# Performance work log

Hardware: AMD Instinct MI355X
Metric: run time of the kernel (lower is better)

The kernel has to match this reference:

```python
import jax, jax.numpy as jnp
import numpy as np

H = 2048   # hidden_size
L = 512    # latent_dim
B, S = 4, 2048

def setup_inputs() -> dict:
    key = jax.random.key(0)
    ks = jax.random.split(key, 13)
    def lin(k, fan_in, shape):
        bound = 1.0 / np.sqrt(fan_in)
        return jax.random.uniform(k, shape, jnp.float32, -bound, bound)
    return {
        "hidden_states": jax.random.normal(ks[0], (B, S, H), jnp.float32),
        "num_reasoning_steps": 8,
        # to_latent: Linear(H, 2L) -> ReLU -> Linear(2L, L)
        "W_enc1": lin(ks[1], H, (2 * L, H)), "b_enc1": lin(ks[2], H, (2 * L,)),
        "W_enc2": lin(ks[3], 2 * L, (L, 2 * L)), "b_enc2": lin(ks[4], 2 * L, (L,)),
        # from_latent: Linear(L, 2L) -> ReLU -> Linear(2L, H)
        "W_dec1": lin(ks[5], L, (2 * L, L)), "b_dec1": lin(ks[6], L, (2 * L,)),
        "W_dec2": lin(ks[7], 2 * L, (H, 2 * L)), "b_dec2": lin(ks[8], 2 * L, (H,)),
        # GRUCell(L, L): weight_ih/hh [3L, L], bias_ih/hh [3L]
        "w_ih": lin(ks[9], L, (3 * L, L)), "w_hh": lin(ks[10], L, (3 * L, L)),
        "b_ih": lin(ks[11], L, (3 * L,)), "b_hh": lin(ks[12], L, (3 * L,)),
    }

def _gru_cell(x, h, w_ih, w_hh, b_ih, b_hh):
    # PyTorch GRUCell semantics
    gi = x @ w_ih.T + b_ih   # [*, 3L]
    gh = h @ w_hh.T + b_hh
    i_r, i_z, i_n = jnp.split(gi, 3, axis=-1)
    h_r, h_z, h_n = jnp.split(gh, 3, axis=-1)
    r = jax.nn.sigmoid(i_r + h_r)
    z = jax.nn.sigmoid(i_z + h_z)
    n = jnp.tanh(i_n + r * h_n)
    return (1.0 - z) * n + z * h

def reference(hidden_states, num_reasoning_steps, W_enc1, b_enc1, W_enc2, b_enc2,
              W_dec1, b_dec1, W_dec2, b_dec2, w_ih, w_hh, b_ih, b_hh):
    # encode to latent
    latent = jax.nn.relu(hidden_states @ W_enc1.T + b_enc1) @ W_enc2.T + b_enc2  # [B,S,L]

    def step(lat, _):
        lat = _gru_cell(lat, lat, w_ih, w_hh, b_ih, b_hh)
        return lat, lat

    latent, traj = jax.lax.scan(step, latent, None, length=num_reasoning_steps)
    # traj: [steps, B, S, L] -> [B, S, steps, L]
    latent_trajectory = jnp.transpose(traj, (1, 2, 0, 3))
    decoded = jax.nn.relu(latent @ W_dec1.T + b_dec1) @ W_dec2.T + b_dec2  # [B,S,H]
    return decoded, latent_trajectory
```

## Files before the change

### kernel.cpp

```cpp
#include <hip/hip_runtime.h>
#include <hip/hip_bf16.h>
#include <cstdint>
#include <cstddef>

#define TOKENS   8192
#define HID      2048
#define LAT      512
#define LAT2     1024
#define GCOLS    2048
#define STEPS    8
#define DEC_ELEMS (TOKENS*HID)

typedef __attribute__((ext_vector_type(8))) __bf16 bf16x8;
typedef __attribute__((ext_vector_type(4))) float  f32x4;

__device__ __forceinline__ unsigned short f32_to_bf16_rne(float f) {
  unsigned int u = __float_as_uint(f);
  unsigned int r = (u + 0x7FFFu + ((u >> 16) & 1u)) >> 16;
  return (unsigned short)r;
}
__device__ __forceinline__ float bf16_to_f32(unsigned short u) {
  return __uint_as_float(((unsigned int)u) << 16);
}

__device__ __forceinline__ float sigmoidf_(float x) {
  if (x >= 0.f) { float e = __expf(-x); return 1.f / (1.f + e); }
  float e = __expf(x); return e / (1.f + e);
}
__device__ __forceinline__ float tanhf_(float x) {
  float ax = fabsf(x);
  float e  = __expf(-2.f * ax);
  float t  = (1.f - e) / (1.f + e);
  return copysignf(t, x);
}

__device__ __forceinline__ void gl_lds16(const void* g, void* l) {
  __builtin_amdgcn_global_load_lds(
      (const __attribute__((address_space(1))) void*)g,
      (__attribute__((address_space(3))) void*)l, 16, 0, 0);
}

__global__ void k_cast(const float* __restrict__ s, unsigned short* __restrict__ d, int n4) {
  int i = blockIdx.x * blockDim.x + threadIdx.x;
  int stride = gridDim.x * blockDim.x;
  for (; i < n4; i += stride) {
    float4 v = ((const float4*)s)[i];
    ushort4 o;
    o.x = f32_to_bf16_rne(v.x);
    o.y = f32_to_bf16_rne(v.y);
    o.z = f32_to_bf16_rne(v.z);
    o.w = f32_to_bf16_rne(v.w);
    ((ushort4*)d)[i] = o;
  }
}

__global__ void k_gru_pack(const float* __restrict__ wih, const float* __restrict__ whh,
                           const float* __restrict__ bih, const float* __restrict__ bhh,
                           unsigned short* __restrict__ Wg, float* __restrict__ biasg) {
  int gc = blockIdx.x;
  int l  = gc >> 2;
  int g  = gc & 3;
  int row = (g == 0) ? l : (g == 1) ? (512 + l) : (1024 + l);
  for (int c = threadIdx.x; c < LAT; c += blockDim.x) {
    float v;
    if (g <= 1)      v = wih[row * LAT + c] + whh[row * LAT + c];
    else if (g == 2) v = wih[row * LAT + c];
    else             v = whh[row * LAT + c];
    Wg[(size_t)gc * LAT + c] = f32_to_bf16_rne(v);
  }
  if (threadIdx.x == 0) {
    float b;
    if (g <= 1)      b = bih[row] + bhh[row];
    else if (g == 2) b = bih[row];
    else             b = bhh[row];
    biasg[gc] = b;
  }
}

#define MWG 128
#define NWG 128
#define KTILE 64

template <int EPI>
__global__ __launch_bounds__(256)
void gemm_bt(const unsigned short* __restrict__ A,
             const unsigned short* __restrict__ W,
             const float* __restrict__ bias,
             int K, int N,
             float* __restrict__ outF,
             unsigned short* __restrict__ outB) {
  __shared__ __align__(16) char smem[2 * MWG * KTILE * 2];
  unsigned short* As = (unsigned short*)smem;
  unsigned short* Bs = As + MWG * KTILE;

  const int tid  = threadIdx.x;
  const int lane = tid & 63;
  const int wv   = tid >> 6;
  const int wr   = wv >> 1;
  const int wc   = wv & 1;
  const int m0   = blockIdx.x * MWG;
  const int n0   = blockIdx.y * NWG;

  const int lr = lane & 15;
  const int lq = lane >> 4;

  const int srow = lane >> 3;
  const int scol = (lane & 7) * 8;

  f32x4 acc[4][4];
#pragma unroll
  for (int i = 0; i < 4; ++i)
#pragma unroll
    for (int j = 0; j < 4; ++j) acc[i][j] = (f32x4){0.f, 0.f, 0.f, 0.f};

  const unsigned short* Ab = A + (size_t)m0 * K;
  const unsigned short* Wb = W + (size_t)n0 * K;

  const int KT = K / KTILE;
  for (int kt = 0; kt < KT; ++kt) {
    const int k0 = kt * KTILE;
#pragma unroll
    for (int q = 0; q < 4; ++q) {
      int row = 32 * wv + 8 * q + srow;
      gl_lds16(Ab + (size_t)row * K + k0 + scol, As + (32 * wv + 8 * q) * KTILE);
      gl_lds16(Wb + (size_t)row * K + k0 + scol, Bs + (32 * wv + 8 * q) * KTILE);
    }
    __syncthreads();
#pragma unroll
    for (int kk = 0; kk < KTILE; kk += 32) {
      bf16x8 af[4], bf[4];
#pragma unroll
      for (int i = 0; i < 4; ++i)
        af[i] = *(const bf16x8*)(As + (wr * 64 + i * 16 + lr) * KTILE + kk + lq * 8);
#pragma unroll
      for (int j = 0; j < 4; ++j)
        bf[j] = *(const bf16x8*)(Bs + (wc * 64 + j * 16 + lr) * KTILE + kk + lq * 8);
#pragma unroll
      for (int i = 0; i < 4; ++i)
#pragma unroll
        for (int j = 0; j < 4; ++j)
          acc[i][j] = __builtin_amdgcn_mfma_f32_16x16x32_bf16(af[i], bf[j], acc[i][j], 0, 0, 0);
    }
    __syncthreads();
  }

  float bj[4];
#pragma unroll
  for (int j = 0; j < 4; ++j) bj[j] = bias[n0 + wc * 64 + j * 16 + lr];
#pragma unroll
  for (int i = 0; i < 4; ++i) {
#pragma unroll
    for (int ii = 0; ii < 4; ++ii) {
      int row = m0 + wr * 64 + i * 16 + 4 * lq + ii;
#pragma unroll
      for (int j = 0; j < 4; ++j) {
        int col = n0 + wc * 64 + j * 16 + lr;
        float v = acc[i][j][ii] + bj[j];
        if constexpr (EPI == 0) {
          outB[(size_t)row * N + col] = f32_to_bf16_rne(fmaxf(v, 0.f));
        } else if constexpr (EPI == 1) {
          outB[(size_t)row * N + col] = f32_to_bf16_rne(v);
        } else {
          outF[(size_t)row * N + col] = v;
        }
      }
    }
  }
}


#define WAIT_LGKM0() asm volatile("s_waitcnt lgkmcnt(0)" ::: "memory")
#define WAIT_VM(n)   asm volatile("s_waitcnt vmcnt(" #n ")" ::: "memory")

#define LOAD_A(buf, mh) { \
  const int baseA = (buf)*65536 + wm*16384; \
  _Pragma("unroll") for (int m4 = 0; m4 < 4; ++m4) \
  _Pragma("unroll") for (int kki = 0; kki < 2; ++kki) { \
    int rl = (mh)*64 + m4*16 + lr; \
    int off = (rl*128 + kki*64 + lq*16) ^ ((rl & 7) << 4); \
    aR[mh][m4][kki] = *(const bf16x8*)(lds_ + baseA + off); } }

#define LOAD_B(buf, nh) { \
  const int baseB = (buf)*65536 + 32768 + (wn >> 1)*16384; \
  _Pragma("unroll") for (int n2 = 0; n2 < 2; ++n2) \
  _Pragma("unroll") for (int kki = 0; kki < 2; ++kki) { \
    int rl = (wn & 1)*64 + ((nh)*2 + n2)*16 + lr; \
    int off = (rl*128 + kki*64 + lq*16) ^ ((rl & 7) << 4); \
    bR[nh][n2][kki] = *(const bf16x8*)(lds_ + baseB + off); } }

#define STAGE_A(buf, half, kt) { \
  const unsigned short* gp = A + (size_t)(m0 + (half)*128 + rr8)*K + (size_t)(kt)*64 + cc8; \
  char* dp = lds_ + (buf)*65536 + (half)*16384 + (wv << 10); \
  gl_lds16(gp, dp); \
  gl_lds16(gp + (size_t)64*K, dp + 8192); }

#define STAGE_B(buf, half, kt) { \
  const unsigned short* gp = W + (size_t)(n0 + (half)*128 + rr8)*K + (size_t)(kt)*64 + cc8; \
  char* dp = lds_ + (buf)*65536 + 32768 + (half)*16384 + (wv << 10); \
  gl_lds16(gp, dp); \
  gl_lds16(gp + (size_t)64*K, dp + 8192); }

#define MFMAQ(mh, nh) \
  _Pragma("unroll") for (int kki = 0; kki < 2; ++kki) \
  _Pragma("unroll") for (int n2 = 0; n2 < 2; ++n2) \
  _Pragma("unroll") for (int m4 = 0; m4 < 4; ++m4) \
    acc[(mh)*4 + m4][(nh)*2 + n2] = __builtin_amdgcn_mfma_f32_16x16x32_bf16( \
        aR[mh][m4][kki], bR[nh][n2][kki], acc[(mh)*4 + m4][(nh)*2 + n2], 0, 0, 0);

#define PH_CORE(mh, nh) \
  __builtin_amdgcn_s_barrier(); \
  WAIT_LGKM0(); \
  __builtin_amdgcn_sched_barrier(0); \
  __builtin_amdgcn_s_setprio(1); \
  MFMAQ(mh, nh); \
  __builtin_amdgcn_sched_barrier(0); \
  __builtin_amdgcn_s_setprio(0);

#define PH_BAR() __builtin_amdgcn_s_barrier();

template <int EPI>
__global__ __launch_bounds__(512, 2)
void gemm256(const unsigned short* __restrict__ A,
             const unsigned short* __restrict__ W,
             const float* __restrict__ bias,
             int K, int N, int Ntiles,
             float* __restrict__ outF,
             unsigned short* __restrict__ outB,
             const unsigned short* __restrict__ hInB,
             float* __restrict__ traj,
             int step) {
  __shared__ __align__(16) char lds_[131072];

  const int tid  = threadIdx.x;
  const int lane = tid & 63;
  const int wv   = tid >> 6;
  const int wm   = wv >> 2;
  const int wn   = wv & 3;
  const int lr   = lane & 15;
  const int lq   = lane >> 4;

  const int rr8 = (wv << 3) + (lane >> 3);
  const int cc8 = ((lane & 7) ^ (lane >> 3)) << 3;

  const int nwg = gridDim.x;
  const int wg  = blockIdx.x;
  const int swz = (wg & 7) * (nwg >> 3) + (wg >> 3);
  const int tm  = swz / Ntiles;
  const int tn  = swz % Ntiles;
  const int m0  = tm * 256;
  const int n0  = tn * 256;

  f32x4 acc[8][4];
#pragma unroll
  for (int i = 0; i < 8; ++i)
#pragma unroll
    for (int j = 0; j < 4; ++j) acc[i][j] = (f32x4){0.f, 0.f, 0.f, 0.f};

  bf16x8 aR[2][4][2];
  bf16x8 bR[2][2][2];

  const int nIt = K >> 7;

  STAGE_B(0, 0, 0) STAGE_B(0, 1, 0) STAGE_A(0, 0, 0) STAGE_A(0, 1, 0)
  STAGE_B(1, 0, 1) STAGE_B(1, 1, 1)
  WAIT_VM(4);
  __builtin_amdgcn_s_barrier();

  for (int t = 0; t < nIt - 1; ++t) {
    const int kt1 = 2 * t + 1;
    const int kt2 = 2 * t + 2;
    const int kt3 = 2 * t + 3;
    LOAD_A(0, 0) LOAD_B(0, 0)
    STAGE_A(1, 0, kt1)
    PH_CORE(0, 0) PH_BAR()
    LOAD_B(0, 1)
    STAGE_A(1, 1, kt1)
    PH_CORE(0, 1) PH_BAR()
    LOAD_A(0, 1)
    STAGE_B(0, 0, kt2)
    PH_CORE(1, 1) PH_BAR()
    STAGE_B(0, 1, kt2)
    PH_CORE(1, 0)
    WAIT_VM(4);
    PH_BAR()
    LOAD_A(1, 0) LOAD_B(1, 0)
    STAGE_A(0, 0, kt2)
    PH_CORE(0, 0) PH_BAR()
    LOAD_B(1, 1)
    STAGE_A(0, 1, kt2)
    PH_CORE(0, 1) PH_BAR()
    LOAD_A(1, 1)
    STAGE_B(1, 0, kt3)
    PH_CORE(1, 1) PH_BAR()
    STAGE_B(1, 1, kt3)
    PH_CORE(1, 0)
    WAIT_VM(4);
    PH_BAR()
  }

  {
    const int ktL = 2 * nIt - 1;
    LOAD_A(0, 0) LOAD_B(0, 0)
    STAGE_A(1, 0, ktL)
    PH_CORE(0, 0) PH_BAR()
    LOAD_B(0, 1)
    STAGE_A(1, 1, ktL)
    PH_CORE(0, 1) PH_BAR()
    LOAD_A(0, 1)
    PH_CORE(1, 1) PH_BAR()
    PH_CORE(1, 0)
    WAIT_VM(0);
    PH_BAR()
    LOAD_A(1, 0) LOAD_B(1, 0)
    PH_CORE(0, 0) PH_BAR()
    LOAD_B(1, 1)
    PH_CORE(0, 1) PH_BAR()
    LOAD_A(1, 1)
    PH_CORE(1, 1) PH_BAR()
    PH_CORE(1, 0)
    PH_BAR()
  }

  float bj[4];
#pragma unroll
  for (int nf = 0; nf < 4; ++nf) bj[nf] = bias[n0 + wn * 64 + nf * 16 + lr];

  if constexpr (EPI == 2) {
#pragma unroll
    for (int mf = 0; mf < 8; ++mf) {
#pragma unroll
      for (int ii = 0; ii < 4; ++ii) {
        int row = m0 + wm * 128 + mf * 16 + lq * 4 + ii;
#pragma unroll
        for (int nf = 0; nf < 4; ++nf) {
          int col = n0 + wn * 64 + nf * 16 + lr;
          outF[(size_t)row * N + col] = acc[mf][nf][ii] + bj[nf];
        }
      }
    }
  } else {
    float* scr = (float*)lds_ + wv * 1088;
    const int latBase = tn * 64 + wn * 16;
    const int la = lane & 15;
    const int th = lane >> 4;
#pragma unroll
    for (int mf = 0; mf < 8; ++mf) {
      WAIT_LGKM0();
#pragma unroll
      for (int nf = 0; nf < 4; ++nf)
#pragma unroll
        for (int ii = 0; ii < 4; ++ii)
          scr[(lq * 4 + ii) * 68 + nf * 16 + lr] = acc[mf][nf][ii] + bj[nf];
      WAIT_LGKM0();
#pragma unroll
      for (int tb = 0; tb < 4; ++tb) {
        int tt = th * 4 + tb;
        int token = m0 + wm * 128 + mf * 16 + tt;
        f32x4 g = *(const f32x4*)(scr + tt * 68 + la * 4);
        int latc = latBase + la;
        float h  = bf16_to_f32(hInB[(size_t)token * LAT + latc]);
        float r  = sigmoidf_(g.x);
        float z  = sigmoidf_(g.y);
        float n  = tanhf_(g.z + r * g.w);
        float hn = (1.f - z) * n + z * h;
        outB[(size_t)token * LAT + latc] = f32_to_bf16_rne(hn);
        traj[(size_t)token * (STEPS * LAT) + step * LAT + latc] = hn;
      }
    }
  }
}

extern "C" void kernel_launch(void* const* d_in, const int* in_sizes, int n_in,
                              void* d_out, int out_size, void* d_ws, size_t ws_size,
                              hipStream_t stream) {
  const float* hs  = (const float*)d_in[0];
  const float* We1 = (const float*)d_in[2];
  const float* be1 = (const float*)d_in[3];
  const float* We2 = (const float*)d_in[4];
  const float* be2 = (const float*)d_in[5];
  const float* Wd1 = (const float*)d_in[6];
  const float* bd1 = (const float*)d_in[7];
  const float* Wd2 = (const float*)d_in[8];
  const float* bd2 = (const float*)d_in[9];
  const float* wih = (const float*)d_in[10];
  const float* whh = (const float*)d_in[11];
  const float* bih = (const float*)d_in[12];
  const float* bhh = (const float*)d_in[13];

  char* ws = (char*)d_ws;
  unsigned short* A0    = (unsigned short*)(ws + 0);
  unsigned short* We1b  = (unsigned short*)(ws + 33554432);
  unsigned short* We2b  = (unsigned short*)(ws + 37748736);
  unsigned short* Wd1b  = (unsigned short*)(ws + 38797312);
  unsigned short* Wd2b  = (unsigned short*)(ws + 39845888);
  unsigned short* Wg    = (unsigned short*)(ws + 44040192);
  float*          biasg = (float*)         (ws + 46137344);
  unsigned short* X1    = (unsigned short*)(ws + 46145536);
  unsigned short* Lb0   = (unsigned short*)(ws + 62922752);
  unsigned short* Lb1   = (unsigned short*)(ws + 71311360);
  unsigned short* X2    = A0;

  float* dec  = (float*)d_out;
  float* traj = (float*)d_out + DEC_ELEMS;

  k_cast<<<2048, 256, 0, stream>>>(hs,  A0,   TOKENS * HID / 4);
  k_cast<<<512,  256, 0, stream>>>(We1, We1b, LAT2 * HID / 4);
  k_cast<<<256,  256, 0, stream>>>(We2, We2b, LAT * LAT2 / 4);
  k_cast<<<256,  256, 0, stream>>>(Wd1, Wd1b, LAT2 * LAT / 4);
  k_cast<<<512,  256, 0, stream>>>(Wd2, Wd2b, HID * LAT2 / 4);
  k_gru_pack<<<GCOLS, 128, 0, stream>>>(wih, whh, bih, bhh, Wg, biasg);

  gemm_bt<0><<<dim3(TOKENS / MWG, LAT2 / NWG), dim3(256), 0, stream>>>(
      A0, We1b, be1, HID, LAT2, nullptr, X1);
  gemm_bt<1><<<dim3(TOKENS / MWG, LAT / NWG), dim3(256), 0, stream>>>(
      X1, We2b, be2, LAT2, LAT, nullptr, Lb0);
  for (int s = 0; s < STEPS; ++s) {
    const unsigned short* lbi = (s & 1) ? Lb1 : Lb0;
    unsigned short*       lbo = (s & 1) ? Lb0 : Lb1;
    gemm256<3><<<256, 512, 0, stream>>>(lbi, Wg, biasg, LAT, GCOLS, 8,
                                        nullptr, lbo, lbi, traj, s);
  }
  gemm_bt<0><<<dim3(TOKENS / MWG, LAT2 / NWG), dim3(256), 0, stream>>>(
      Lb0, Wd1b, bd1, LAT, LAT2, nullptr, X2);
  gemm256<2><<<256, 512, 0, stream>>>(X2, Wd2b, bd2, LAT2, HID, 8,
                                      dec, nullptr, nullptr, nullptr, 0);
}
```

Before: 440.0 us.

## Fuse GRU steps into one persistent kernel with grid barrier and merge casts

The eight per-step GRU GEMM launches become a single persistent kernel. It loops over the steps and uses an atomic counter in workspace as a grid-wide barrier, and it prefetches the weight tiles for the next step before waiting. The five separate fp32-to-bf16 cast launches are merged into one kernel that dispatches by index range. This targets launch overhead and the pipeline drain and refill between steps, but it depends on all 256 workgroups being resident at once and adds spin-wait cost.

```diff
diff --git a/kernel.cpp b/kernel.cpp
--- a/kernel.cpp
+++ b/kernel.cpp
@@ -40,17 +40,29 @@
       (__attribute__((address_space(3))) void*)l, 16, 0, 0);
 }
 
-__global__ void k_cast(const float* __restrict__ s, unsigned short* __restrict__ d, int n4) {
+__global__ void k_prep(const float* __restrict__ hs,  const float* __restrict__ We1,
+                       const float* __restrict__ We2, const float* __restrict__ Wd1,
+                       const float* __restrict__ Wd2,
+                       unsigned short* __restrict__ A0,   unsigned short* __restrict__ We1b,
+                       unsigned short* __restrict__ We2b, unsigned short* __restrict__ Wd1b,
+                       unsigned short* __restrict__ Wd2b) {
+  const int total = 5505024;
   int i = blockIdx.x * blockDim.x + threadIdx.x;
   int stride = gridDim.x * blockDim.x;
-  for (; i < n4; i += stride) {
-    float4 v = ((const float4*)s)[i];
+  for (; i < total; i += stride) {
+    const float* s; unsigned short* d; int j;
+    if (i < 4194304)      { s = hs;  d = A0;   j = i; }
+    else if (i < 4718592) { s = We1; d = We1b; j = i - 4194304; }
+    else if (i < 4849664) { s = We2; d = We2b; j = i - 4718592; }
+    else if (i < 4980736) { s = Wd1; d = Wd1b; j = i - 4849664; }
+    else                  { s = Wd2; d = Wd2b; j = i - 4980736; }
+    float4 v = ((const float4*)s)[j];
     ushort4 o;
     o.x = f32_to_bf16_rne(v.x);
     o.y = f32_to_bf16_rne(v.y);
     o.z = f32_to_bf16_rne(v.z);
     o.w = f32_to_bf16_rne(v.w);
-    ((ushort4*)d)[i] = o;
+    ((ushort4*)d)[j] = o;
   }
 }
 
@@ -87,7 +99,6 @@
              const unsigned short* __restrict__ W,
              const float* __restrict__ bias,
              int K, int N,
-             float* __restrict__ outF,
              unsigned short* __restrict__ outB) {
   __shared__ __align__(16) char smem[2 * MWG * KTILE * 2];
   unsigned short* As = (unsigned short*)smem;
@@ -158,10 +169,8 @@
         float v = acc[i][j][ii] + bj[j];
         if constexpr (EPI == 0) {
           outB[(size_t)row * N + col] = f32_to_bf16_rne(fmaxf(v, 0.f));
-        } else if constexpr (EPI == 1) {
+        } else {
           outB[(size_t)row * N + col] = f32_to_bf16_rne(v);
-        } else {
-          outF[(size_t)row * N + col] = v;
         }
       }
     }
@@ -218,17 +227,64 @@
 
 #define PH_BAR() __builtin_amdgcn_s_barrier();
 
-template <int EPI>
+#define KLOOP_MAIN(tlim) \
+  for (int t = 0; t < (tlim); ++t) { \
+    const int kt1 = 2 * t + 1, kt2 = 2 * t + 2, kt3 = 2 * t + 3; \
+    LOAD_A(0, 0) LOAD_B(0, 0) \
+    STAGE_A(1, 0, kt1) \
+    PH_CORE(0, 0) PH_BAR() \
+    LOAD_B(0, 1) \
+    STAGE_A(1, 1, kt1) \
+    PH_CORE(0, 1) PH_BAR() \
+    LOAD_A(0, 1) \
+    STAGE_B(0, 0, kt2) \
+    PH_CORE(1, 1) PH_BAR() \
+    STAGE_B(0, 1, kt2) \
+    PH_CORE(1, 0) \
+    WAIT_VM(4); \
+    PH_BAR() \
+    LOAD_A(1, 0) LOAD_B(1, 0) \
+    STAGE_A(0, 0, kt2) \
+    PH_CORE(0, 0) PH_BAR() \
+    LOAD_B(1, 1) \
+    STAGE_A(0, 1, kt2) \
+    PH_CORE(0, 1) PH_BAR() \
+    LOAD_A(1, 1) \
+    STAGE_B(1, 0, kt3) \
+    PH_CORE(1, 1) PH_BAR() \
+    STAGE_B(1, 1, kt3) \
+    PH_CORE(1, 0) \
+    WAIT_VM(4); \
+    PH_BAR() \
+  }
+
+#define KLOOP_LAST(ktL) { \
+    LOAD_A(0, 0) LOAD_B(0, 0) \
+    STAGE_A(1, 0, (ktL)) \
+    PH_CORE(0, 0) PH_BAR() \
+    LOAD_B(0, 1) \
+    STAGE_A(1, 1, (ktL)) \
+    PH_CORE(0, 1) PH_BAR() \
+    LOAD_A(0, 1) \
+    PH_CORE(1, 1) PH_BAR() \
+    PH_CORE(1, 0) \
+    WAIT_VM(0); \
+    PH_BAR() \
+    LOAD_A(1, 0) LOAD_B(1, 0) \
+    PH_CORE(0, 0) PH_BAR() \
+    LOAD_B(1, 1) \
+    PH_CORE(0, 1) PH_BAR() \
+    LOAD_A(1, 1) \
+    PH_CORE(1, 1) PH_BAR() \
+    PH_CORE(1, 0) \
+    PH_BAR() \
+  }
+
 __global__ __launch_bounds__(512, 2)
-void gemm256(const unsigned short* __restrict__ A,
-             const unsigned short* __restrict__ W,
-             const float* __restrict__ bias,
-             int K, int N, int Ntiles,
-             float* __restrict__ outF,
-             unsigned short* __restrict__ outB,
-             const unsigned short* __restrict__ hInB,
-             float* __restrict__ traj,
-             int step) {
+void gemm256_f(const unsigned short* __restrict__ A,
+               const unsigned short* __restrict__ W,
+               const float* __restrict__ bias, int K, int N, int Ntiles,
+               float* __restrict__ outF) {
   __shared__ __align__(16) char lds_[131072];
 
   const int tid  = threadIdx.x;
@@ -238,7 +294,6 @@
   const int wn   = wv & 3;
   const int lr   = lane & 15;
   const int lq   = lane >> 4;
-
   const int rr8 = (wv << 3) + (lane >> 3);
   const int cc8 = ((lane & 7) ^ (lane >> 3)) << 3;
 
@@ -266,106 +321,130 @@
   WAIT_VM(4);
   __builtin_amdgcn_s_barrier();
 
-  for (int t = 0; t < nIt - 1; ++t) {
-    const int kt1 = 2 * t + 1;
-    const int kt2 = 2 * t + 2;
-    const int kt3 = 2 * t + 3;
-    LOAD_A(0, 0) LOAD_B(0, 0)
-    STAGE_A(1, 0, kt1)
-    PH_CORE(0, 0) PH_BAR()
-    LOAD_B(0, 1)
-    STAGE_A(1, 1, kt1)
-    PH_CORE(0, 1) PH_BAR()
-    LOAD_A(0, 1)
-    STAGE_B(0, 0, kt2)
-    PH_CORE(1, 1) PH_BAR()
-    STAGE_B(0, 1, kt2)
-    PH_CORE(1, 0)
-    WAIT_VM(4);
-    PH_BAR()
-    LOAD_A(1, 0) LOAD_B(1, 0)
-    STAGE_A(0, 0, kt2)
-    PH_CORE(0, 0) PH_BAR()
-    LOAD_B(1, 1)
-    STAGE_A(0, 1, kt2)
-    PH_CORE(0, 1) PH_BAR()
-    LOAD_A(1, 1)
-    STAGE_B(1, 0, kt3)
-    PH_CORE(1, 1) PH_BAR()
-    STAGE_B(1, 1, kt3)
-    PH_CORE(1, 0)
-    WAIT_VM(4);
-    PH_BAR()
-  }
-
-  {
-    const int ktL = 2 * nIt - 1;
-    LOAD_A(0, 0) LOAD_B(0, 0)
-    STAGE_A(1, 0, ktL)
-    PH_CORE(0, 0) PH_BAR()
-    LOAD_B(0, 1)
-    STAGE_A(1, 1, ktL)
-    PH_CORE(0, 1) PH_BAR()
-    LOAD_A(0, 1)
-    PH_CORE(1, 1) PH_BAR()
-    PH_CORE(1, 0)
-    WAIT_VM(0);
-    PH_BAR()
-    LOAD_A(1, 0) LOAD_B(1, 0)
-    PH_CORE(0, 0) PH_BAR()
-    LOAD_B(1, 1)
-    PH_CORE(0, 1) PH_BAR()
-    LOAD_A(1, 1)
-    PH_CORE(1, 1) PH_BAR()
-    PH_CORE(1, 0)
-    PH_BAR()
-  }
+  KLOOP_MAIN(nIt - 1)
+  KLOOP_LAST(2 * nIt - 1)
 
   float bj[4];
 #pragma unroll
   for (int nf = 0; nf < 4; ++nf) bj[nf] = bias[n0 + wn * 64 + nf * 16 + lr];
-
-  if constexpr (EPI == 2) {
-#pragma unroll
-    for (int mf = 0; mf < 8; ++mf) {
-#pragma unroll
-      for (int ii = 0; ii < 4; ++ii) {
-        int row = m0 + wm * 128 + mf * 16 + lq * 4 + ii;
-#pragma unroll
-        for (int nf = 0; nf < 4; ++nf) {
-          int col = n0 + wn * 64 + nf * 16 + lr;
-          outF[(size_t)row * N + col] = acc[mf][nf][ii] + bj[nf];
+#pragma unroll
+  for (int mf = 0; mf < 8; ++mf) {
+#pragma unroll
+    for (int ii = 0; ii < 4; ++ii) {
+      int row = m0 + wm * 128 + mf * 16 + lq * 4 + ii;
+#pragma unroll
+      for (int nf = 0; nf < 4; ++nf) {
+        int col = n0 + wn * 64 + nf * 16 + lr;
+        outF[(size_t)row * N + col] = acc[mf][nf][ii] + bj[nf];
+      }
+    }
+  }
+}
+
+__global__ __launch_bounds__(512, 2)
+void gru_fused(unsigned short* __restrict__ h0,
+               unsigned short* __restrict__ h1,
+               const unsigned short* __restrict__ Wg,
+               const float* __restrict__ biasg,
+               float* __restrict__ traj,
+               unsigned int* __restrict__ bar) {
+  __shared__ __align__(16) char lds_[131072];
+
+  const int tid  = threadIdx.x;
+  const int lane = tid & 63;
+  const int wv   = tid >> 6;
+  const int wm   = wv >> 2;
+  const int wn   = wv & 3;
+  const int lr   = lane & 15;
+  const int lq   = lane >> 4;
+  const int rr8 = (wv << 3) + (lane >> 3);
+  const int cc8 = ((lane & 7) ^ (lane >> 3)) << 3;
+
+  const int K = LAT;
+  const unsigned short* W = Wg;
+
+  const int nwg = gridDim.x;
+  const int wg  = blockIdx.x;
+  const int swz = (wg & 7) * (nwg >> 3) + (wg >> 3);
+  const int tm  = swz >> 3;
+  const int tn  = swz & 7;
+  const int m0  = tm * 256;
+  const int n0  = tn * 256;
+
+  bf16x8 aR[2][4][2];
+  bf16x8 bR[2][2][2];
+
+  float bj[4];
+#pragma unroll
+  for (int nf = 0; nf < 4; ++nf) bj[nf] = biasg[n0 + wn * 64 + nf * 16 + lr];
+
+  const unsigned short* A = h0;
+
+  STAGE_B(0, 0, 0) STAGE_B(0, 1, 0) STAGE_A(0, 0, 0) STAGE_A(0, 1, 0)
+  STAGE_B(1, 0, 1) STAGE_B(1, 1, 1)
+  WAIT_VM(4);
+  __builtin_amdgcn_s_barrier();
+
+  for (int s = 0; s < STEPS; ++s) {
+    unsigned short* hout = (s & 1) ? h0 : h1;
+
+    f32x4 acc[8][4];
+#pragma unroll
+    for (int i = 0; i < 8; ++i)
+#pragma unroll
+      for (int j = 0; j < 4; ++j) acc[i][j] = (f32x4){0.f, 0.f, 0.f, 0.f};
+
+    KLOOP_MAIN(3)
+    KLOOP_LAST(7)
+
+    {
+      float* scr = (float*)lds_ + wv * 1088;
+      const int latBase = tn * 64 + wn * 16;
+      const int la = lane & 15;
+      const int th = lane >> 4;
+#pragma unroll
+      for (int mf = 0; mf < 8; ++mf) {
+        WAIT_LGKM0();
+#pragma unroll
+        for (int nf = 0; nf < 4; ++nf)
+#pragma unroll
+          for (int ii = 0; ii < 4; ++ii)
+            scr[(lq * 4 + ii) * 68 + nf * 16 + lr] = acc[mf][nf][ii] + bj[nf];
+        WAIT_LGKM0();
+#pragma unroll
+        for (int tb = 0; tb < 4; ++tb) {
+          int tt = th * 4 + tb;
+          int token = m0 + wm * 128 + mf * 16 + tt;
+          f32x4 g = *(const f32x4*)(scr + tt * 68 + la * 4);
+          int latc = latBase + la;
+          float h  = bf16_to_f32(A[(size_t)token * LAT + latc]);
+          float r  = sigmoidf_(g.x);
+          float z  = sigmoidf_(g.y);
+          float n  = tanhf_(g.z + r * g.w);
+          float hn = (1.f - z) * n + z * h;
+          hout[(size_t)token * LAT + latc] = f32_to_bf16_rne(hn);
+          traj[(size_t)token * (STEPS * LAT) + s * LAT + latc] = hn;
         }
       }
     }
-  } else {
-    float* scr = (float*)lds_ + wv * 1088;
-    const int latBase = tn * 64 + wn * 16;
-    const int la = lane & 15;
-    const int th = lane >> 4;
-#pragma unroll
-    for (int mf = 0; mf < 8; ++mf) {
-      WAIT_LGKM0();
-#pragma unroll
-      for (int nf = 0; nf < 4; ++nf)
-#pragma unroll
-        for (int ii = 0; ii < 4; ++ii)
-          scr[(lq * 4 + ii) * 68 + nf * 16 + lr] = acc[mf][nf][ii] + bj[nf];
-      WAIT_LGKM0();
-#pragma unroll
-      for (int tb = 0; tb < 4; ++tb) {
-        int tt = th * 4 + tb;
-        int token = m0 + wm * 128 + mf * 16 + tt;
-        f32x4 g = *(const f32x4*)(scr + tt * 68 + la * 4);
-        int latc = latBase + la;
-        float h  = bf16_to_f32(hInB[(size_t)token * LAT + latc]);
-        float r  = sigmoidf_(g.x);
-        float z  = sigmoidf_(g.y);
-        float n  = tanhf_(g.z + r * g.w);
-        float hn = (1.f - z) * n + z * h;
-        outB[(size_t)token * LAT + latc] = f32_to_bf16_rne(hn);
-        traj[(size_t)token * (STEPS * LAT) + step * LAT + latc] = hn;
+
+    if (s < STEPS - 1) {
+      __threadfence();
+      __syncthreads();
+      STAGE_B(0, 0, 0) STAGE_B(0, 1, 0)
+      if (tid == 0) {
+        __hip_atomic_fetch_add(bar, 1u, __ATOMIC_RELEASE, __HIP_MEMORY_SCOPE_AGENT);
+        unsigned int target = 256u * (unsigned)(s + 1);
+        while (__hip_atomic_load(bar, __ATOMIC_RELAXED, __HIP_MEMORY_SCOPE_AGENT) < target)
+          __builtin_amdgcn_s_sleep(1);
       }
+      __syncthreads();
+      __threadfence();
+      A = (s & 1) ? h0 : h1;
+      STAGE_A(0, 0, 0) STAGE_A(0, 1, 0)
+      STAGE_B(1, 0, 1) STAGE_B(1, 1, 1)
+      WAIT_VM(4);
+      __builtin_amdgcn_s_barrier();
     }
   }
 }
@@ -398,30 +477,22 @@
   unsigned short* X1    = (unsigned short*)(ws + 46145536);
   unsigned short* Lb0   = (unsigned short*)(ws + 62922752);
   unsigned short* Lb1   = (unsigned short*)(ws + 71311360);
+  unsigned int*   bar   = (unsigned int*)  (ws + 79699968);
   unsigned short* X2    = A0;
 
   float* dec  = (float*)d_out;
   float* traj = (float*)d_out + DEC_ELEMS;
 
-  k_cast<<<2048, 256, 0, stream>>>(hs,  A0,   TOKENS * HID / 4);
-  k_cast<<<512,  256, 0, stream>>>(We1, We1b, LAT2 * HID / 4);
-  k_cast<<<256,  256, 0, stream>>>(We2, We2b, LAT * LAT2 / 4);
-  k_cast<<<256,  256, 0, stream>>>(Wd1, Wd1b, LAT2 * LAT / 4);
-  k_cast<<<512,  256, 0, stream>>>(Wd2, Wd2b, HID * LAT2 / 4);
+  hipMemsetAsync(bar, 0, 4, stream);
+  k_prep<<<2048, 256, 0, stream>>>(hs, We1, We2, Wd1, Wd2, A0, We1b, We2b, Wd1b, Wd2b);
   k_gru_pack<<<GCOLS, 128, 0, stream>>>(wih, whh, bih, bhh, Wg, biasg);
 
   gemm_bt<0><<<dim3(TOKENS / MWG, LAT2 / NWG), dim3(256), 0, stream>>>(
-      A0, We1b, be1, HID, LAT2, nullptr, X1);
+      A0, We1b, be1, HID, LAT2, X1);
   gemm_bt<1><<<dim3(TOKENS / MWG, LAT / NWG), dim3(256), 0, stream>>>(
-      X1, We2b, be2, LAT2, LAT, nullptr, Lb0);
-  for (int s = 0; s < STEPS; ++s) {
-    const unsigned short* lbi = (s & 1) ? Lb1 : Lb0;
-    unsigned short*       lbo = (s & 1) ? Lb0 : Lb1;
-    gemm256<3><<<256, 512, 0, stream>>>(lbi, Wg, biasg, LAT, GCOLS, 8,
-                                        nullptr, lbo, lbi, traj, s);
-  }
+      X1, We2b, be2, LAT2, LAT, Lb0);
+  gru_fused<<<256, 512, 0, stream>>>(Lb0, Lb1, Wg, biasg, traj, bar);
   gemm_bt<0><<<dim3(TOKENS / MWG, LAT2 / NWG), dim3(256), 0, stream>>>(
-      Lb0, Wd1b, bd1, LAT, LAT2, nullptr, X2);
-  gemm256<2><<<256, 512, 0, stream>>>(X2, Wd2b, bd2, LAT2, HID, 8,
-                                      dec, nullptr, nullptr, nullptr, 0);
-}
+      Lb0, Wd1b, bd1, LAT, LAT2, X2);
+  gemm256_f<<<256, 512, 0, stream>>>(X2, Wd2b, bd2, LAT2, HID, 8, dec);
+}
```

Result: slower. 1.498 ms (+240.4%).
